# Optimization experiments

Measured on AMD Instinct MI355X. Metric: run time of the kernel, lower is better.

The kernel has to match this reference:

```python
import jax, jax.numpy as jnp
import numpy as np

GAMMA, LMBD, EPS = 0.99, 0.95, 0.2
T, D, H, A = 262144, 128, 256, 8


def _mlp_gauss(x, W1, b1, Wmu, bmu, Wlv, blv):
    h = jnp.tanh(x @ W1 + b1)
    return h @ Wmu + bmu, h @ Wlv + blv  # mu, logvar: [T, A]


def _critic(x, Wc1, bc1, Wc2, bc2):
    h = jnp.tanh(x @ Wc1 + bc1)
    return h @ Wc2 + bc2  # [T, 1]


def setup_inputs() -> dict:
    key = jax.random.key(0)
    ks = jax.random.split(key, 12)
    s = 0.05  # small init scale for stable exp()/ratio
    return {
        "state": jax.random.normal(ks[0], (T, D), jnp.float32),
        "next_state": jax.random.normal(ks[1], (T, D), jnp.float32),
        "action": jax.random.normal(ks[2], (T, A), jnp.float32),
        "beta_log_prob": jax.random.normal(ks[3], (T, A), jnp.float32) * 0.1,
        "reward": jax.random.normal(ks[4], (T,), jnp.float32),
        "W1": jax.random.normal(ks[5], (D, H), jnp.float32) * s,
        "b1": jnp.zeros((H,), jnp.float32),
        "Wmu": jax.random.normal(ks[6], (H, A), jnp.float32) * s,
        "bmu": jnp.zeros((A,), jnp.float32),
        "Wlv": jax.random.normal(ks[7], (H, A), jnp.float32) * s,
        "blv": jnp.zeros((A,), jnp.float32),
        "Wc1": jax.random.normal(ks[8], (D, H), jnp.float32) * s,
        "bc1": jnp.zeros((H,), jnp.float32),
        "Wc2": jax.random.normal(ks[9], (H, 1), jnp.float32) * s,
        "bc2": jnp.zeros((1,), jnp.float32),
    }


def reference(state, next_state, action, beta_log_prob, reward,
              W1, b1, Wmu, bmu, Wlv, blv, Wc1, bc1, Wc2, bc2):
    # critic values
    value = _critic(state, Wc1, bc1, Wc2, bc2)            # [T, 1]
    v0 = value[:, 0]                                       # [T]
    v1 = _critic(next_state, Wc1, bc1, Wc2, bc2)[:, 0]     # [T]

    # GAE: reverse recurrence gae_t = delta_t + gamma*lambda*gae_{t+1}
    delta = reward + GAMMA * v1 - v0                       # [T]

    def step(g, d):
        g = d + GAMMA * LMBD * g
        return g, g

    _, gae_rev = jax.lax.scan(step, jnp.float32(0.0), delta[::-1])
    # torch code rebuilds each gae into a fresh Tensor -> returns are detached
    ret = jax.lax.stop_gradient(gae_rev[::-1][:, None])    # [T, 1]

    advantage = ret - value                                # [T, 1] (grad via value)
    a_hat = (advantage - advantage.mean()) / (jnp.std(advantage, ddof=1) + 1e-7)

    # pi log-prob of actions under Normal(mu, sqrt(exp(logvar)))
    mu, logvar = _mlp_gauss(state, W1, b1, Wmu, bmu, Wlv, blv)  # [T, A]
    log_2pi = jnp.float32(np.log(2.0 * np.pi))
    pi_lp = -0.5 * ((action - mu) ** 2) * jnp.exp(-logvar) - 0.5 * logvar - 0.5 * log_2pi

    ratio = jnp.exp(jnp.sum(pi_lp - jax.lax.stop_gradient(beta_log_prob),
                            axis=1, keepdims=True))        # [T, 1]

    actor_loss = -jnp.sum(jnp.minimum(ratio * a_hat,
                                      jnp.clip(ratio, 1.0 - EPS, 1.0 + EPS) * a_hat))
    critic_loss = jnp.sum(advantage ** 2)
    return actor_loss + critic_loss
```

## Files before the change

### kernel.cpp

```cpp
#include <hip/hip_runtime.h>

#define T_N   262144
#define D_IN  128
#define A_DIM 8
#define GAMMA 0.99f
#define EPS_C 0.2f
#define C_GL  0.9405f
#define HALF_LOG_2PI 0.9189385332f
#define SCALE2 2.8853900817779268f
#define ST_TPB 8
#define NX_TPB 4
#define HB_S   20

typedef __attribute__((ext_vector_type(8))) short short8;
typedef __attribute__((ext_vector_type(4))) float f32x4;

__device__ __forceinline__ unsigned short f2bf(float f) {
  unsigned int u = __float_as_uint(f);
  u += 0x7FFFu + ((u >> 16) & 1u);
  return (unsigned short)(u >> 16);
}
__device__ __forceinline__ unsigned int pack_bf2(float lo, float hi) {
  return __builtin_amdgcn_perm(__float_as_uint(hi), __float_as_uint(lo), 0x07060302u);
}
__device__ __forceinline__ unsigned short bf_trunc(float f) {
  return (unsigned short)(__float_as_uint(f) >> 16);
}
__device__ __forceinline__ float tanh_pre(float a) {
  float e = __builtin_amdgcn_exp2f(a);
  return 1.f - 2.f * __builtin_amdgcn_rcpf(e + 1.f);
}
template <int CTRL>
__device__ __forceinline__ float dpp_add(float p) {
  return p + __int_as_float(__builtin_amdgcn_update_dpp(
                 0, __float_as_int(p), CTRL, 0xF, 0xF, true));
}
__device__ __forceinline__ float row16_sum(float p) {
  p = dpp_add<0x111>(p); p = dpp_add<0x112>(p);
  p = dpp_add<0x114>(p); p = dpp_add<0x118>(p);
  return p;
}
__device__ __forceinline__ float xor8_sum(float p) {
  p = dpp_add<0xB1>(p); p = dpp_add<0x4E>(p); p = dpp_add<0x141>(p);
  return p;
}

__global__ __launch_bounds__(256) void k_prep(
    const float* __restrict__ Wc1, const float* __restrict__ W1,
    const float* __restrict__ Wmu, const float* __restrict__ Wlv,
    unsigned short* __restrict__ Wc1Ts, unsigned short* __restrict__ W1Ts,
    unsigned short* __restrict__ H1, float* __restrict__ accs) {
  int i = blockIdx.x * 256 + threadIdx.x;
  if (blockIdx.x == 0 && threadIdx.x < 8) ((unsigned int*)accs)[threadIdx.x] = 0u;
  if (i < 32768) {
    int n = i >> 7, k = i & 127;
    Wc1Ts[i] = f2bf(Wc1[k * 256 + n] * SCALE2);
  } else if (i < 65536) {
    int j = i - 32768; int n = j >> 7, k = j & 127;
    W1Ts[j] = f2bf(W1[k * 256 + n] * SCALE2);
  } else if (i < 69632) {
    int j = i - 65536; int h = j >> 8, n = j & 255;
    H1[j] = (h < 8) ? f2bf(Wmu[n * 8 + h]) : f2bf(Wlv[n * 8 + (h - 8)]);
  }
}

__global__ __launch_bounds__(512, 4) void k_state(
    const float* __restrict__ state,
    const float* __restrict__ action, const float* __restrict__ beta_lp,
    const unsigned short* __restrict__ Wc1Ts, const unsigned short* __restrict__ W1Ts,
    const unsigned short* __restrict__ H1,
    const float* __restrict__ bc1, const float* __restrict__ b1,
    const float* __restrict__ Wc2, const float* __restrict__ bc2,
    const float* __restrict__ bmu, const float* __restrict__ blv,
    float* __restrict__ v0out, float* __restrict__ ratio) {
  const int tid  = threadIdx.x;
  const int lane = tid & 63;
  const int wv   = tid >> 6;
  const int role = wv >> 2;
  const int wl   = wv & 3;
  const int c    = lane & 15;
  const int quad = lane >> 4;

  __shared__ unsigned short sh_x[32 * 136];
  __shared__ unsigned short sh_h[32 * 264];
  __shared__ float sh_hb[4 * 32 * HB_S];
  __shared__ float sh_v[32 * 4];

  const unsigned short* WT = role ? W1Ts : Wc1Ts;
  const float* bias = role ? b1 : bc1;

  short8 bfrag[4][4];
  float bias_c[4], wc2_c[4];
#pragma unroll
  for (int ct = 0; ct < 4; ++ct) {
    int n = wl * 64 + ct * 16 + c;
    bias_c[ct] = bias[n] * SCALE2;
    wc2_c[ct]  = Wc2[n];
#pragma unroll
    for (int ki = 0; ki < 4; ++ki)
      bfrag[ct][ki] = *(const short8*)(WT + n * 128 + ki * 32 + quad * 8);
  }
  const float vbias = bc2[0];
  const int aa = tid & 7;
  const float bmu_a = bmu[aa], blv_a = blv[aa];

  const int t0 = blockIdx.x * ST_TPB;

  float4 rbuf[2];
  {
    const float4* Xv = (const float4*)(state + (size_t)t0 * 32 * D_IN);
    rbuf[0] = Xv[tid]; rbuf[1] = Xv[tid + 512];
  }

  for (int i = 0; i < ST_TPB; ++i) {
    const int r0 = (t0 + i) * 32;

#pragma unroll
    for (int j = 0; j < 2; ++j) {
      int e4 = tid + j * 512;
      int row = e4 >> 5, c4 = e4 & 31;
      uint2 u;
      u.x = pack_bf2(rbuf[j].x, rbuf[j].y);
      u.y = pack_bf2(rbuf[j].z, rbuf[j].w);
      *(uint2*)(&sh_x[row * 136 + c4 * 4]) = u;
    }
    __syncthreads();

    if (i + 1 < ST_TPB) {
      const float4* Xv2 = (const float4*)(state + (size_t)(r0 + 32) * D_IN);
      rbuf[0] = Xv2[tid]; rbuf[1] = Xv2[tid + 512];
    }
    float fa = 0.f, fb = 0.f;
    if (tid < 256) { fa = action[r0 * 8 + tid]; fb = beta_lp[r0 * 8 + tid]; }

    if (role == 0) {
#pragma unroll
      for (int rt = 0; rt < 2; ++rt) {
        f32x4 acc[4];
#pragma unroll
        for (int ct = 0; ct < 4; ++ct) acc[ct] = (f32x4){0.f, 0.f, 0.f, 0.f};
#pragma unroll
        for (int ki = 0; ki < 4; ++ki) {
          short8 a = *(const short8*)(&sh_x[(rt * 16 + c) * 136 + ki * 32 + quad * 8]);
#pragma unroll
          for (int ct = 0; ct < 4; ++ct)
            acc[ct] = __builtin_amdgcn_mfma_f32_16x16x32_bf16(a, bfrag[ct][ki], acc[ct], 0, 0, 0);
        }
#pragma unroll
        for (int r = 0; r < 4; ++r) {
          float p = 0.f;
#pragma unroll
          for (int ct = 0; ct < 4; ++ct)
            p += tanh_pre(acc[ct][r] + bias_c[ct]) * wc2_c[ct];
          p = row16_sum(p);
          if (c == 15) sh_v[(rt * 16 + quad * 4 + r) * 4 + wl] = p;
        }
      }
    } else {
#pragma unroll
      for (int rt = 0; rt < 2; ++rt) {
        f32x4 acc[4];
#pragma unroll
        for (int ct = 0; ct < 4; ++ct) acc[ct] = (f32x4){0.f, 0.f, 0.f, 0.f};
#pragma unroll
        for (int ki = 0; ki < 4; ++ki) {
          short8 a = *(const short8*)(&sh_x[(rt * 16 + c) * 136 + ki * 32 + quad * 8]);
#pragma unroll
          for (int ct = 0; ct < 4; ++ct)
            acc[ct] = __builtin_amdgcn_mfma_f32_16x16x32_bf16(a, bfrag[ct][ki], acc[ct], 0, 0, 0);
        }
#pragma unroll
        for (int ct = 0; ct < 4; ++ct) {
          int col = wl * 64 + ct * 16 + c;
#pragma unroll
          for (int r = 0; r < 4; ++r) {
            int row = rt * 16 + quad * 4 + r;
            sh_h[row * 264 + col] = bf_trunc(tanh_pre(acc[ct][r] + bias_c[ct]));
          }
        }
      }
    }
    __syncthreads();

    if (role == 1) {
#pragma unroll
      for (int st = 0; st < 2; ++st) {
        f32x4 acc2 = (f32x4){0.f, 0.f, 0.f, 0.f};
#pragma unroll
        for (int k2 = 0; k2 < 2; ++k2) {
          int kofs = wl * 64 + k2 * 32 + quad * 8;
          short8 a2 = *(const short8*)(H1 + c * 256 + kofs);
          short8 b2 = *(const short8*)(&sh_h[(st * 16 + c) * 264 + kofs]);
          acc2 = __builtin_amdgcn_mfma_f32_16x16x32_bf16(a2, b2, acc2, 0, 0, 0);
        }
        *((f32x4*)&sh_hb[((wl * 32) + st * 16 + c) * HB_S + quad * 4]) = acc2;
      }
    } else if (tid < 32) {
      v0out[r0 + tid] = sh_v[tid * 4] + sh_v[tid * 4 + 1] + sh_v[tid * 4 + 2] +
                        sh_v[tid * 4 + 3] + vbias;
    }
    __syncthreads();

    if (tid < 256) {
      int s = tid >> 3;
      float mu = sh_hb[(s)*HB_S + aa]            + sh_hb[(32 + s) * HB_S + aa] +
                 sh_hb[(64 + s) * HB_S + aa]     + sh_hb[(96 + s) * HB_S + aa] + bmu_a;
      float lv = sh_hb[(s)*HB_S + 8 + aa]        + sh_hb[(32 + s) * HB_S + 8 + aa] +
                 sh_hb[(64 + s) * HB_S + 8 + aa] + sh_hb[(96 + s) * HB_S + 8 + aa] + blv_a;
      float d = fa - mu;
      float term = -0.5f * d * d * __expf(-lv) - 0.5f * lv - HALF_LOG_2PI - fb;
      term = xor8_sum(term);
      if (aa == 0) ratio[r0 + s] = __expf(term);
    }
  }
}

__global__ __launch_bounds__(256, 4) void k_next(
    const float* __restrict__ next_state,
    const unsigned short* __restrict__ Wc1Ts,
    const float* __restrict__ bc1, const float* __restrict__ Wc2,
    const float* __restrict__ bc2, float* __restrict__ v1out) {
  const int tid = threadIdx.x;
  const int lane = tid & 63;
  const int wv   = tid >> 6;
  const int c    = lane & 15;
  const int quad = lane >> 4;

  __shared__ unsigned short sh_x[32 * 136];
  __shared__ float sh_v[32 * 4];

  short8 bfrag[4][4];
  float bias_c[4], wc2_c[4];
#pragma unroll
  for (int ct = 0; ct < 4; ++ct) {
    int n = wv * 64 + ct * 16 + c;
    bias_c[ct] = bc1[n] * SCALE2;
    wc2_c[ct]  = Wc2[n];
#pragma unroll
    for (int ki = 0; ki < 4; ++ki)
      bfrag[ct][ki] = *(const short8*)(Wc1Ts + n * 128 + ki * 32 + quad * 8);
  }
  const float vbias = bc2[0];

  const int t0 = blockIdx.x * NX_TPB;
  float4 rbuf[4];
  {
    const float4* Xv = (const float4*)(next_state + (size_t)t0 * 32 * D_IN);
#pragma unroll
    for (int j = 0; j < 4; ++j) rbuf[j] = Xv[tid + j * 256];
  }

  for (int i = 0; i < NX_TPB; ++i) {
    const int r0 = (t0 + i) * 32;
#pragma unroll
    for (int j = 0; j < 4; ++j) {
      int e = tid + j * 256;
      int row = e >> 5, c4 = e & 31;
      uint2 u;
      u.x = pack_bf2(rbuf[j].x, rbuf[j].y);
      u.y = pack_bf2(rbuf[j].z, rbuf[j].w);
      *(uint2*)(&sh_x[row * 136 + c4 * 4]) = u;
    }
    __syncthreads();

    if (i + 1 < NX_TPB) {
      const float4* Xv2 = (const float4*)(next_state + (size_t)(r0 + 32) * D_IN);
#pragma unroll
      for (int j = 0; j < 4; ++j) rbuf[j] = Xv2[tid + j * 256];
    }

#pragma unroll
    for (int rt = 0; rt < 2; ++rt) {
      f32x4 acc[4];
#pragma unroll
      for (int ct = 0; ct < 4; ++ct) acc[ct] = (f32x4){0.f, 0.f, 0.f, 0.f};
#pragma unroll
      for (int ki = 0; ki < 4; ++ki) {
        short8 a = *(const short8*)(&sh_x[(rt * 16 + c) * 136 + ki * 32 + quad * 8]);
#pragma unroll
        for (int ct = 0; ct < 4; ++ct)
          acc[ct] = __builtin_amdgcn_mfma_f32_16x16x32_bf16(a, bfrag[ct][ki], acc[ct], 0, 0, 0);
      }
#pragma unroll
      for (int r = 0; r < 4; ++r) {
        float p = 0.f;
#pragma unroll
        for (int ct = 0; ct < 4; ++ct)
          p += tanh_pre(acc[ct][r] + bias_c[ct]) * wc2_c[ct];
        p = row16_sum(p);
        if (c == 15) sh_v[(rt * 16 + quad * 4 + r) * 4 + wv] = p;
      }
    }
    __syncthreads();
    if (tid < 32) {
      v1out[r0 + tid] = sh_v[tid * 4] + sh_v[tid * 4 + 1] + sh_v[tid * 4 + 2] +
                        sh_v[tid * 4 + 3] + vbias;
    }
  }
}

__global__ __launch_bounds__(256) void k_gae2(
    const float* __restrict__ reward, const float* __restrict__ v0,
    const float* __restrict__ v1, const float* __restrict__ ratio,
    float* __restrict__ accs, float* __restrict__ out) {
  const int j = blockIdx.x, k = threadIdx.x;
  const int base = j * 1024 + k * 8;
  unsigned int* cnt1 = (unsigned int*)accs + 4;
  unsigned int* cnt2 = (unsigned int*)accs + 5;

  float d[8];
  float s = 0.f, w = 1.f;
#pragma unroll
  for (int i = 0; i < 8; ++i) {
    int idx = base + i;
    float dd = 0.f;
    if (idx < T_N) dd = reward[idx] + GAMMA * v1[idx] - v0[idx];
    d[i] = dd;
    s += w * dd;
    w *= C_GL;
  }
  const float W8 = w;
  __shared__ float Ss[256], Sw[256];
  __shared__ float sh_stats[2];
  Ss[k] = s; Sw[k] = W8;
  __syncthreads();
  for (int st = 1; st < 256; st <<= 1) {
    bool has = (k + st) < 256;
    float ns = 0.f, nw = 0.f;
    if (has) { ns = Ss[k] + Sw[k] * Ss[k + st]; nw = Sw[k] * Sw[k + st]; }
    __syncthreads();
    if (has) { Ss[k] = ns; Sw[k] = nw; }
    __syncthreads();
  }
  float g = (k < 255) ? Ss[k + 1] : 0.f;
  float adv[8];
  float sa = 0.f, sq = 0.f;
  if (k < 128) {
#pragma unroll
    for (int i = 7; i >= 0; --i) {
      g = d[i] + C_GL * g;
      float a = g - v0[base + i];
      adv[i] = a;
      sa += a; sq += a * a;
    }
  }
  __syncthreads();
  Ss[k] = sa; Sw[k] = sq;
  __syncthreads();
  for (int off = 128; off > 0; off >>= 1) {
    if (k < off) { Ss[k] += Ss[k + off]; Sw[k] += Sw[k + off]; }
    __syncthreads();
  }
  if (k == 0) {
    atomicAdd(&accs[0], Ss[0]);
    atomicAdd(&accs[1], Sw[0]);
    __hip_atomic_fetch_add(cnt1, 1u, __ATOMIC_RELEASE, __HIP_MEMORY_SCOPE_AGENT);
    while (__hip_atomic_load(cnt1, __ATOMIC_RELAXED, __HIP_MEMORY_SCOPE_AGENT) < 256u)
      __builtin_amdgcn_s_sleep(16);
    (void)__hip_atomic_load(cnt1, __ATOMIC_ACQUIRE, __HIP_MEMORY_SCOPE_AGENT);
    sh_stats[0] = __hip_atomic_load(&accs[0], __ATOMIC_RELAXED, __HIP_MEMORY_SCOPE_AGENT);
    sh_stats[1] = __hip_atomic_load(&accs[1], __ATOMIC_RELAXED, __HIP_MEMORY_SCOPE_AGENT);
  }
  __syncthreads();

  const float sum  = sh_stats[0];
  const float cl   = sh_stats[1];
  const float mean = sum * (1.f / (float)T_N);
  const float var  = (cl - sum * mean) / (float)(T_N - 1);
  const float inv  = 1.f / (sqrtf(var) + 1e-7f);
  float sl = 0.f;
  if (k < 128) {
#pragma unroll
    for (int i = 0; i < 8; ++i) {
      float a = (adv[i] - mean) * inv;
      float r = ratio[base + i];
      float rc = fminf(fmaxf(r, 1.f - EPS_C), 1.f + EPS_C);
      sl += -fminf(r * a, rc * a);
    }
  }
  __syncthreads();
  Ss[k] = sl;
  __syncthreads();
  for (int off = 128; off > 0; off >>= 1) {
    if (k < off) Ss[k] += Ss[k + off];
    __syncthreads();
  }
  if (k == 0) {
    atomicAdd(&accs[2], Ss[0]);
    unsigned int old = __hip_atomic_fetch_add(cnt2, 1u, __ATOMIC_ACQ_REL,
                                              __HIP_MEMORY_SCOPE_AGENT);
    if (old == 255u) {
      float al = __hip_atomic_load(&accs[2], __ATOMIC_RELAXED, __HIP_MEMORY_SCOPE_AGENT);
      out[0] = al + cl;
    }
  }
}

extern "C" void kernel_launch(void* const* d_in, const int* in_sizes, int n_in,
                              void* d_out, int out_size, void* d_ws, size_t ws_size,
                              hipStream_t stream) {
  const float* state      = (const float*)d_in[0];
  const float* next_state = (const float*)d_in[1];
  const float* action     = (const float*)d_in[2];
  const float* beta_lp    = (const float*)d_in[3];
  const float* reward     = (const float*)d_in[4];
  const float* W1   = (const float*)d_in[5];
  const float* b1   = (const float*)d_in[6];
  const float* Wmu  = (const float*)d_in[7];
  const float* bmu  = (const float*)d_in[8];
  const float* Wlv  = (const float*)d_in[9];
  const float* blv  = (const float*)d_in[10];
  const float* Wc1  = (const float*)d_in[11];
  const float* bc1  = (const float*)d_in[12];
  const float* Wc2  = (const float*)d_in[13];
  const float* bc2  = (const float*)d_in[14];

  char* ws = (char*)d_ws;
  size_t o = 0;
  unsigned short* Wc1Ts = (unsigned short*)(ws + o); o += 65536;
  unsigned short* W1Ts  = (unsigned short*)(ws + o); o += 65536;
  unsigned short* H1    = (unsigned short*)(ws + o); o += 8192;
  float* v0    = (float*)(ws + o); o += (size_t)T_N * 4;
  float* v1    = (float*)(ws + o); o += (size_t)T_N * 4;
  float* ratio = (float*)(ws + o); o += (size_t)T_N * 4;
  float* accs  = (float*)(ws + o); o += 256;

  k_prep<<<272, 256, 0, stream>>>(Wc1, W1, Wmu, Wlv, Wc1Ts, W1Ts, H1, accs);

  k_state<<<(T_N / 32) / ST_TPB, 512, 0, stream>>>(
      state, action, beta_lp, Wc1Ts, W1Ts, H1, bc1, b1, Wc2, bc2, bmu, blv,
      v0, ratio);
  k_next<<<(T_N / 32) / NX_TPB, 256, 0, stream>>>(
      next_state, Wc1Ts, bc1, Wc2, bc2, v1);
  k_gae2<<<256, 256, 0, stream>>>(reward, v0, v1, ratio, accs, (float*)d_out);
}
```

Baseline: 374.1 us.

## Fuse next-state critic pass into the state kernel as a second phase

Merges the separate next_state critic kernel into the state kernel. After the state phase, each 512-thread block processes 64-row tiles of next_state, with both wave groups running the critic MLP and the actor-role waves reloading Wc1 fragments. Shared memory is carved from one aliased buffer so the second phase reuses the first phase's storage. This removes one launch and the tail gap between kernels, but the block now runs both phases serially, and NX_TPB (4) with 64 rows per iteration must cover next_state exactly once across the grid.

```diff
diff --git a/kernel.cpp b/kernel.cpp
--- a/kernel.cpp
+++ b/kernel.cpp
@@ -64,15 +64,16 @@
   }
 }
 
-__global__ __launch_bounds__(512, 4) void k_state(
-    const float* __restrict__ state,
+__global__ __launch_bounds__(512, 4) void k_main(
+    const float* __restrict__ state, const float* __restrict__ next_state,
     const float* __restrict__ action, const float* __restrict__ beta_lp,
     const unsigned short* __restrict__ Wc1Ts, const unsigned short* __restrict__ W1Ts,
     const unsigned short* __restrict__ H1,
     const float* __restrict__ bc1, const float* __restrict__ b1,
     const float* __restrict__ Wc2, const float* __restrict__ bc2,
     const float* __restrict__ bmu, const float* __restrict__ blv,
-    float* __restrict__ v0out, float* __restrict__ ratio) {
+    float* __restrict__ v0out, float* __restrict__ v1out,
+    float* __restrict__ ratio) {
   const int tid  = threadIdx.x;
   const int lane = tid & 63;
   const int wv   = tid >> 6;
@@ -81,10 +82,13 @@
   const int c    = lane & 15;
   const int quad = lane >> 4;
 
-  __shared__ unsigned short sh_x[32 * 136];
-  __shared__ unsigned short sh_h[32 * 264];
-  __shared__ float sh_hb[4 * 32 * HB_S];
-  __shared__ float sh_v[32 * 4];
+  __shared__ __align__(16) char smem[36352];
+  unsigned short* sh_x  = (unsigned short*)smem;
+  unsigned short* sh_h  = (unsigned short*)(smem + 8704);
+  float*          sh_hb = (float*)(smem + 25600);
+  float*          sh_v  = (float*)(smem + 35840);
+  unsigned short* sh_x2 = (unsigned short*)smem;
+  float*          sh_v2 = (float*)(smem + 17408);
 
   const unsigned short* WT = role ? W1Ts : Wc1Ts;
   const float* bias = role ? b1 : bc1;
@@ -213,60 +217,45 @@
       if (aa == 0) ratio[r0 + s] = __expf(term);
     }
   }
-}
-
-__global__ __launch_bounds__(256, 4) void k_next(
-    const float* __restrict__ next_state,
-    const unsigned short* __restrict__ Wc1Ts,
-    const float* __restrict__ bc1, const float* __restrict__ Wc2,
-    const float* __restrict__ bc2, float* __restrict__ v1out) {
-  const int tid = threadIdx.x;
-  const int lane = tid & 63;
-  const int wv   = tid >> 6;
-  const int c    = lane & 15;
-  const int quad = lane >> 4;
-
-  __shared__ unsigned short sh_x[32 * 136];
-  __shared__ float sh_v[32 * 4];
-
-  short8 bfrag[4][4];
-  float bias_c[4], wc2_c[4];
-#pragma unroll
-  for (int ct = 0; ct < 4; ++ct) {
-    int n = wv * 64 + ct * 16 + c;
-    bias_c[ct] = bc1[n] * SCALE2;
-    wc2_c[ct]  = Wc2[n];
-#pragma unroll
-    for (int ki = 0; ki < 4; ++ki)
-      bfrag[ct][ki] = *(const short8*)(Wc1Ts + n * 128 + ki * 32 + quad * 8);
-  }
-  const float vbias = bc2[0];
-
-  const int t0 = blockIdx.x * NX_TPB;
-  float4 rbuf[4];
+
+  const int wg  = wv >> 2;
+  const int t0n = blockIdx.x * NX_TPB;
+
+  float4 rbuf2[4];
   {
-    const float4* Xv = (const float4*)(next_state + (size_t)t0 * 32 * D_IN);
-#pragma unroll
-    for (int j = 0; j < 4; ++j) rbuf[j] = Xv[tid + j * 256];
+    const float4* Xv = (const float4*)(next_state + (size_t)t0n * 64 * D_IN);
+#pragma unroll
+    for (int j = 0; j < 4; ++j) rbuf2[j] = Xv[tid + j * 512];
+  }
+  if (role == 1) {
+#pragma unroll
+    for (int ct = 0; ct < 4; ++ct) {
+      int n = wl * 64 + ct * 16 + c;
+      bias_c[ct] = bc1[n] * SCALE2;
+      wc2_c[ct]  = Wc2[n];
+#pragma unroll
+      for (int ki = 0; ki < 4; ++ki)
+        bfrag[ct][ki] = *(const short8*)(Wc1Ts + n * 128 + ki * 32 + quad * 8);
+    }
   }
 
   for (int i = 0; i < NX_TPB; ++i) {
-    const int r0 = (t0 + i) * 32;
+    const int r0 = (t0n + i) * 64;
 #pragma unroll
     for (int j = 0; j < 4; ++j) {
-      int e = tid + j * 256;
-      int row = e >> 5, c4 = e & 31;
+      int e4 = tid + j * 512;
+      int row = e4 >> 5, c4 = e4 & 31;
       uint2 u;
-      u.x = pack_bf2(rbuf[j].x, rbuf[j].y);
-      u.y = pack_bf2(rbuf[j].z, rbuf[j].w);
-      *(uint2*)(&sh_x[row * 136 + c4 * 4]) = u;
+      u.x = pack_bf2(rbuf2[j].x, rbuf2[j].y);
+      u.y = pack_bf2(rbuf2[j].z, rbuf2[j].w);
+      *(uint2*)(&sh_x2[row * 136 + c4 * 4]) = u;
     }
     __syncthreads();
 
     if (i + 1 < NX_TPB) {
-      const float4* Xv2 = (const float4*)(next_state + (size_t)(r0 + 32) * D_IN);
-#pragma unroll
-      for (int j = 0; j < 4; ++j) rbuf[j] = Xv2[tid + j * 256];
+      const float4* Xv2 = (const float4*)(next_state + (size_t)(r0 + 64) * D_IN);
+#pragma unroll
+      for (int j = 0; j < 4; ++j) rbuf2[j] = Xv2[tid + j * 512];
     }
 
 #pragma unroll
@@ -276,7 +265,7 @@
       for (int ct = 0; ct < 4; ++ct) acc[ct] = (f32x4){0.f, 0.f, 0.f, 0.f};
 #pragma unroll
       for (int ki = 0; ki < 4; ++ki) {
-        short8 a = *(const short8*)(&sh_x[(rt * 16 + c) * 136 + ki * 32 + quad * 8]);
+        short8 a = *(const short8*)(&sh_x2[(wg * 32 + rt * 16 + c) * 136 + ki * 32 + quad * 8]);
 #pragma unroll
         for (int ct = 0; ct < 4; ++ct)
           acc[ct] = __builtin_amdgcn_mfma_f32_16x16x32_bf16(a, bfrag[ct][ki], acc[ct], 0, 0, 0);
@@ -288,14 +277,14 @@
         for (int ct = 0; ct < 4; ++ct)
           p += tanh_pre(acc[ct][r] + bias_c[ct]) * wc2_c[ct];
         p = row16_sum(p);
-        if (c == 15) sh_v[(rt * 16 + quad * 4 + r) * 4 + wv] = p;
+        if (c == 15) sh_v2[(wg * 32 + rt * 16 + quad * 4 + r) * 4 + wl] = p;
       }
     }
     __syncthreads();
-    if (tid < 32) {
-      v1out[r0 + tid] = sh_v[tid * 4] + sh_v[tid * 4 + 1] + sh_v[tid * 4 + 2] +
-                        sh_v[tid * 4 + 3] + vbias;
-    }
+
+    if (tid < 64)
+      v1out[r0 + tid] = sh_v2[tid * 4] + sh_v2[tid * 4 + 1] + sh_v2[tid * 4 + 2] +
+                        sh_v2[tid * 4 + 3] + vbias;
   }
 }
 
@@ -427,10 +416,9 @@
 
   k_prep<<<272, 256, 0, stream>>>(Wc1, W1, Wmu, Wlv, Wc1Ts, W1Ts, H1, accs);
 
-  k_state<<<(T_N / 32) / ST_TPB, 512, 0, stream>>>(
-      state, action, beta_lp, Wc1Ts, W1Ts, H1, bc1, b1, Wc2, bc2, bmu, blv,
-      v0, ratio);
-  k_next<<<(T_N / 32) / NX_TPB, 256, 0, stream>>>(
-      next_state, Wc1Ts, bc1, Wc2, bc2, v1);
+  k_main<<<(T_N / 32) / ST_TPB, 512, 0, stream>>>(
+      state, next_state, action, beta_lp, Wc1Ts, W1Ts, H1,
+      bc1, b1, Wc2, bc2, bmu, blv, v0, v1, ratio);
+
   k_gae2<<<256, 256, 0, stream>>>(reward, v0, v1, ratio, accs, (float*)d_out);
 }
```

New measurement: 398.5 us. 6.5% more time.
